# Performance work log

Measured on AMD Instinct MI355X. Metric: run time of the kernel, lower is better.

The kernel has to match this reference:

```python
import jax, jax.numpy as jnp
import numpy as np

B, L, S = 4, 1024, 1024
D_MODEL, H, DK = 1024, 16, 64  # d_model == H * DK required by the in-place writeback


def setup_inputs() -> dict:
    key = jax.random.key(0)
    ks = jax.random.split(key, 12)
    queries = jax.random.normal(ks[0], (B, L, D_MODEL), dtype=jnp.float32)
    keys = jax.random.normal(ks[1], (B, S, D_MODEL), dtype=jnp.float32)
    values = jax.random.normal(ks[2], (B, S, D_MODEL), dtype=jnp.float32)
    gate_scores = jax.random.uniform(ks[3], (B, H, DK, D_MODEL), dtype=jnp.float32)
    sc = 1.0 / np.sqrt(D_MODEL)
    W_q = jax.random.normal(ks[4], (H * DK, D_MODEL), dtype=jnp.float32) * sc
    b_q = jax.random.normal(ks[5], (H * DK,), dtype=jnp.float32) * 0.01
    W_k = jax.random.normal(ks[6], (H * DK, D_MODEL), dtype=jnp.float32) * sc
    b_k = jax.random.normal(ks[7], (H * DK,), dtype=jnp.float32) * 0.01
    W_v = jax.random.normal(ks[8], (H * DK, D_MODEL), dtype=jnp.float32) * sc
    b_v = jax.random.normal(ks[9], (H * DK,), dtype=jnp.float32) * 0.01
    W_o = jax.random.normal(ks[10], (D_MODEL, H * DK), dtype=jnp.float32) * sc
    b_o = jax.random.normal(ks[11], (D_MODEL,), dtype=jnp.float32) * 0.01
    return {"queries": queries, "keys": keys, "values": values,
            "gate_scores": gate_scores, "W_q": W_q, "b_q": b_q,
            "W_k": W_k, "b_k": b_k, "W_v": W_v, "b_v": b_v,
            "W_o": W_o, "b_o": b_o}


def reference(queries, keys, values, gate_scores, W_q, b_q, W_k, b_k, W_v, b_v, W_o, b_o):
    # Per-sample gated Q/K/V projection: W_x[b] = gate_scores[b] * W_x  (elementwise, [H,DK,Dm])
    # fused as a batched einsum instead of the per-sample Python loop.
    Wq = W_q.reshape(H, DK, D_MODEL)
    Wk = W_k.reshape(H, DK, D_MODEL)
    Wv = W_v.reshape(H, DK, D_MODEL)
    Q = jnp.einsum('blm,bhkm,hkm->blhk', queries, gate_scores, Wq) + b_q.reshape(H, DK)
    K = jnp.einsum('bsm,bhkm,hkm->bshk', keys, gate_scores, Wk) + b_k.reshape(H, DK)
    V = jnp.einsum('bsm,bhkm,hkm->bshk', values, gate_scores, Wv) + b_v.reshape(H, DK)
    # Full scaled dot-product attention (standard inner_attention)
    scale = 1.0 / jnp.sqrt(jnp.asarray(DK, Q.dtype))
    scores = jnp.einsum('blhk,bshk->bhls', Q, K) * scale
    attn = jax.nn.softmax(scores, axis=-1)
    out = jnp.einsum('bhls,bshk->blhk', attn, V).reshape(B, L, H * DK)
    out = out @ W_o.T + b_o
    return out, attn
```

## Files before the change

kernel.cpp:

```cpp
#include <hip/hip_runtime.h>
#include <math.h>

#define BB 4
#define LL 1024
#define SS 1024
#define DM 1024
#define HH 16
#define DKH 64
#define NH 1024
#define QK_ALPHA 0.1803368801f

typedef __attribute__((ext_vector_type(8))) short bf16x8;
typedef __attribute__((ext_vector_type(4))) float f32x4;
typedef unsigned short ushort_t;
typedef unsigned int uint_t;

#define MFMA16(a, b, c) __builtin_amdgcn_mfma_f32_16x16x32_bf16((a), (b), (c), 0, 0, 0)

__device__ __forceinline__ ushort_t f2b(float f) {
    union { float f; uint_t u; } x; x.f = f;
    uint_t r = x.u + 0x7fffu + ((x.u >> 16) & 1u);
    return (ushort_t)(r >> 16);
}

__device__ __forceinline__ float b2f(ushort_t v) {
    union { float f; uint_t u; } x; x.u = ((uint_t)v) << 16;
    return x.f;
}

__device__ __forceinline__ void gload_lds16(const void* g, void* l) {
    __builtin_amdgcn_global_load_lds(
        (const __attribute__((address_space(1))) unsigned int*)g,
        (__attribute__((address_space(3))) unsigned int*)l, 16, 0, 0);
}

__device__ __forceinline__ int xcd_swz(int lin, int nwg) {
    return (lin & 7) * (nwg >> 3) + (lin >> 3);
}

__device__ __forceinline__ void cvt8(const float* src, ushort_t* dst, const float* g2) {
    float4 a  = *(const float4*)(src);
    float4 b4 = *(const float4*)(src + 4);
    if (g2) {
        float4 ga = *(const float4*)(g2);
        float4 gb = *(const float4*)(g2 + 4);
        a.x *= ga.x; a.y *= ga.y; a.z *= ga.z; a.w *= ga.w;
        b4.x *= gb.x; b4.y *= gb.y; b4.z *= gb.z; b4.w *= gb.w;
    }
    uint4 o;
    o.x = f2b(a.x)  | ((uint_t)f2b(a.y)  << 16);
    o.y = f2b(a.z)  | ((uint_t)f2b(a.w)  << 16);
    o.z = f2b(b4.x) | ((uint_t)f2b(b4.y) << 16);
    o.w = f2b(b4.z) | ((uint_t)f2b(b4.w) << 16);
    *(uint4*)dst = o;
}

__global__ __launch_bounds__(256) void prep_kernel(
    const float* __restrict__ q, const float* __restrict__ k, const float* __restrict__ v,
    const float* __restrict__ gate,
    const float* __restrict__ Wq, const float* __restrict__ Wk, const float* __restrict__ Wv,
    const float* __restrict__ Wo,
    ushort_t* __restrict__ Xq, ushort_t* __restrict__ Xk, ushort_t* __restrict__ Xv,
    ushort_t* __restrict__ Gq, ushort_t* __restrict__ Gk, ushort_t* __restrict__ Gv,
    ushort_t* __restrict__ Wo2)
{
    const int XCH = 3 * 524288;
    const int GCH = 524288;
    const int WCH = 131072;
    for (int c = blockIdx.x * 256 + threadIdx.x; c < XCH + GCH + WCH; c += gridDim.x * 256) {
        if (c < XCH) {
            int r = c >> 19;
            int e = (c & 524287) * 8;
            cvt8((r == 0 ? q : r == 1 ? k : v) + e,
                 (r == 0 ? Xq : r == 1 ? Xk : Xv) + e, nullptr);
        } else if (c < XCH + GCH) {
            int e = (c - XCH) * 8;
            int nm = e & 1048575;
            const float* g2 = gate + e;
            cvt8(Wq + nm, Gq + e, g2);
            cvt8(Wk + nm, Gk + e, g2);
            cvt8(Wv + nm, Gv + e, g2);
        } else {
            int e = (c - XCH - GCH) * 8;
            cvt8(Wo + e, Wo2 + e, nullptr);
        }
    }
}

__global__ __launch_bounds__(256) void qkv_gemm(
    const ushort_t* __restrict__ Xq, const ushort_t* __restrict__ Gq, const float* __restrict__ bq,
    const ushort_t* __restrict__ Xk, const ushort_t* __restrict__ Gk, const float* __restrict__ bk,
    const ushort_t* __restrict__ Xv, const ushort_t* __restrict__ Gv, const float* __restrict__ bv,
    ushort_t* __restrict__ Qb, ushort_t* __restrict__ Kb, ushort_t* __restrict__ Vt,
    int mode)
{
    __shared__ ushort_t As[128 * 64];
    __shared__ ushort_t Bs[128 * 64];
    const int p  = xcd_swz(blockIdx.x, gridDim.x);
    const int g2 = p >> 6;
    const int r  = p & 63;
    int b, g;
    if (mode == 0)      { b = g2 / 3;  g = g2 % 3; }
    else if (mode == 1) { b = g2 >> 1; g = g2 & 1; }
    else                { b = g2;      g = 2;      }
    const size_t off = (size_t)b * 1048576;
    const ushort_t *A, *B; const float* bias; ushort_t* C; bool brow;
    if (g == 0)      { A = Xq + off; B = Gq + off; bias = bq; C = Qb + off; brow = false; }
    else if (g == 1) { A = Xk + off; B = Gk + off; bias = bk; C = Kb + off; brow = false; }
    else             { A = Gv + off; B = Xv + off; bias = bv; C = Vt + off; brow = true;  }
    const float oscale = (g == 0) ? QK_ALPHA : 1.0f;

    const int bm = (r >> 3) * 128;
    const int bn = (r & 7) * 128;
    const int tid = threadIdx.x;
    const int lane = tid & 63;
    const int w = tid >> 6;
    const int wr = w >> 1, wc = w & 1;
    const int lr = lane & 15, lk = lane >> 4;

    f32x4 acc[4][4];
    #pragma unroll
    for (int i = 0; i < 4; ++i)
        #pragma unroll
        for (int j = 0; j < 4; ++j)
            acc[i][j] = (f32x4){0.f, 0.f, 0.f, 0.f};

    for (int k0 = 0; k0 < 1024; k0 += 64) {
        #pragma unroll
        for (int pp = 0; pp < 4; ++pp) {
            int f = pp * 256 + tid;
            int row = f >> 3, seg = f & 7;
            int kb2 = (seg * 8) ^ ((row & 7) * 8);
            gload_lds16(A + (size_t)(bm + row) * 1024 + k0 + kb2,
                        (char*)As + ((pp * 256 + (w << 6)) << 4));
            gload_lds16(B + (size_t)(bn + row) * 1024 + k0 + kb2,
                        (char*)Bs + ((pp * 256 + (w << 6)) << 4));
        }
        __syncthreads();
        #pragma unroll
        for (int kk = 0; kk < 2; ++kk) {
            bf16x8 af[4], bfr[4];
            #pragma unroll
            for (int i = 0; i < 4; ++i) {
                int row = wr * 64 + i * 16 + lr;
                af[i] = *(const bf16x8*)&As[row * 64 + ((lk * 8 + kk * 32) ^ ((row & 7) * 8))];
            }
            #pragma unroll
            for (int j = 0; j < 4; ++j) {
                int row = wc * 64 + j * 16 + lr;
                bfr[j] = *(const bf16x8*)&Bs[row * 64 + ((lk * 8 + kk * 32) ^ ((row & 7) * 8))];
            }
            #pragma unroll
            for (int i = 0; i < 4; ++i)
                #pragma unroll
                for (int j = 0; j < 4; ++j)
                    acc[i][j] = MFMA16(af[i], bfr[j], acc[i][j]);
        }
        __syncthreads();
    }

    #pragma unroll
    for (int i = 0; i < 4; ++i)
        #pragma unroll
        for (int j = 0; j < 4; ++j)
            #pragma unroll
            for (int rr = 0; rr < 4; ++rr) {
                int row = bm + wr * 64 + i * 16 + lk * 4 + rr;
                int col = bn + wc * 64 + j * 16 + lr;
                float vv = (acc[i][j][rr] + bias[brow ? row : col]) * oscale;
                C[(size_t)row * 1024 + col] = f2b(vv);
            }
}

__global__ __launch_bounds__(512) void fused_attn_kernel(
    const ushort_t* __restrict__ Q, const ushort_t* __restrict__ Kmat,
    const ushort_t* __restrict__ Vt, float* __restrict__ attn,
    ushort_t* __restrict__ ctx)
{
    __shared__ ushort_t K2[2][128 * 64];
    __shared__ ushort_t V2[2][64 * 128];
    __shared__ ushort_t Ps[8 * 1024];
    const int p  = xcd_swz(blockIdx.x, gridDim.x);
    const int bh = p >> 3;
    const int b  = bh >> 4;
    const int h  = bh & 15;
    const int r0 = (p & 7) * 128;
    const int tid = threadIdx.x, lane = tid & 63, w = tid >> 6;
    const int lr = lane & 15, lk = lane >> 4;

    bf16x8 aq[2];
    {
        const ushort_t* Qrow = Q + ((size_t)b * LL + r0 + w * 16 + lr) * NH + h * DKH;
        aq[0] = *(const bf16x8*)(Qrow + lk * 8);
        aq[1] = *(const bf16x8*)(Qrow + lk * 8 + 32);
    }
    const ushort_t* Kp = Kmat + (size_t)b * SS * NH + h * DKH;
    const ushort_t* Vp = Vt + ((size_t)b * NH + h * DKH) * SS;
    ushort_t* Psw = Ps + w * 1024;

    const int srow = tid >> 3;
    const int sseg = tid & 7;
    const int skb  = (sseg * 8) ^ ((srow & 7) * 8);
    const int vrow = tid >> 4;
    const int vseg = tid & 15;
    const int vkb  = (vseg * 8) ^ ((vrow & 7) * 8);

#define STAGE_K(t, buf)                                                          \
    do {                                                                         \
        gload_lds16(Kp + (size_t)((t) * 128 + srow) * NH + skb,                  \
                    (char*)(&K2[buf][0]) + (w << 10));                           \
        gload_lds16(Kp + (size_t)((t) * 128 + 64 + srow) * NH + skb,             \
                    (char*)(&K2[buf][0]) + 8192 + (w << 10));                    \
    } while (0)
#define STAGE_V(t, buf)                                                          \
    do {                                                                         \
        gload_lds16(Vp + (size_t)vrow * SS + (t) * 128 + vkb,                    \
                    (char*)(&V2[buf][0]) + (w << 10));                           \
        gload_lds16(Vp + (size_t)(vrow + 32) * SS + (t) * 128 + vkb,             \
                    (char*)(&V2[buf][0]) + 8192 + (w << 10));                    \
    } while (0)

    float inv[4] = {0.f, 0.f, 0.f, 0.f};

    STAGE_K(0, 0);
    __syncthreads();
    for (int t = 0; t < 8; ++t) {
        const int cur = t & 1;
        if (t < 7) STAGE_K(t + 1, cur ^ 1);
        #pragma unroll
        for (int jh = 0; jh < 2; ++jh) {
            f32x4 acc[4];
            #pragma unroll
            for (int j = 0; j < 4; ++j) acc[j] = (f32x4){0.f, 0.f, 0.f, 0.f};
            #pragma unroll
            for (int kk = 0; kk < 2; ++kk)
                #pragma unroll
                for (int j = 0; j < 4; ++j) {
                    int row = jh * 64 + j * 16 + lr;
                    bf16x8 bk2 = *(const bf16x8*)&K2[cur][row * 64 + ((lk * 8 + kk * 32) ^ ((row & 7) * 8))];
                    acc[j] = MFMA16(aq[kk], bk2, acc[j]);
                }
            #pragma unroll
            for (int rr = 0; rr < 4; ++rr)
                inv[rr] += __builtin_amdgcn_exp2f(acc[0][rr]) + __builtin_amdgcn_exp2f(acc[1][rr])
                         + __builtin_amdgcn_exp2f(acc[2][rr]) + __builtin_amdgcn_exp2f(acc[3][rr]);
        }
        __syncthreads();
    }
    #pragma unroll
    for (int rr = 0; rr < 4; ++rr) {
        float s = inv[rr];
        s += __shfl_xor(s, 1);
        s += __shfl_xor(s, 2);
        s += __shfl_xor(s, 4);
        s += __shfl_xor(s, 8);
        inv[rr] = 1.0f / s;
    }

    f32x4 occ[4];
    #pragma unroll
    for (int j = 0; j < 4; ++j) occ[j] = (f32x4){0.f, 0.f, 0.f, 0.f};
    float* Ob = attn + (((size_t)b * HH + h) * LL + r0 + w * 16) * SS;
    const int erow = lane >> 3;
    const int eseg = lane & 7;

    STAGE_K(0, 0);
    STAGE_V(0, 0);
    __syncthreads();
    for (int t = 0; t < 8; ++t) {
        const int cur = t & 1;
        if (t < 7) { STAGE_K(t + 1, cur ^ 1); STAGE_V(t + 1, cur ^ 1); }
        #pragma unroll
        for (int jh = 0; jh < 2; ++jh) {
            f32x4 acc[4];
            #pragma unroll
            for (int j = 0; j < 4; ++j) acc[j] = (f32x4){0.f, 0.f, 0.f, 0.f};
            #pragma unroll
            for (int kk = 0; kk < 2; ++kk)
                #pragma unroll
                for (int j = 0; j < 4; ++j) {
                    int row = jh * 64 + j * 16 + lr;
                    bf16x8 bk2 = *(const bf16x8*)&K2[cur][row * 64 + ((lk * 8 + kk * 32) ^ ((row & 7) * 8))];
                    acc[j] = MFMA16(aq[kk], bk2, acc[j]);
                }
            #pragma unroll
            for (int j = 0; j < 4; ++j)
                #pragma unroll
                for (int rr = 0; rr < 4; ++rr) {
                    int ql = lk * 4 + rr;
                    float pv = __builtin_amdgcn_exp2f(acc[j][rr]) * inv[rr];
                    Psw[ql * 64 + ((j * 16 + lr) ^ ((ql & 7) * 8))] = f2b(pv);
                }
            #pragma unroll
            for (int kk = 0; kk < 2; ++kk) {
                bf16x8 pa = *(const bf16x8*)&Psw[lr * 64 + ((kk * 32 + lk * 8) ^ ((lr & 7) * 8))];
                #pragma unroll
                for (int j = 0; j < 4; ++j) {
                    int row = j * 16 + lr;
                    bf16x8 bv2 = *(const bf16x8*)&V2[cur][row * 128 + ((jh * 64 + kk * 32 + lk * 8) ^ ((row & 7) * 8))];
                    occ[j] = MFMA16(pa, bv2, occ[j]);
                }
            }
            float* Obt = Ob + t * 128 + jh * 64;
            #pragma unroll
            for (int hh = 0; hh < 2; ++hh) {
                int rl = erow + hh * 8;
                bf16x8 p8 = *(const bf16x8*)&Psw[rl * 64 + ((eseg * 8) ^ ((rl & 7) * 8))];
                float4 o0 = make_float4(b2f((ushort_t)p8[0]), b2f((ushort_t)p8[1]),
                                        b2f((ushort_t)p8[2]), b2f((ushort_t)p8[3]));
                float4 o1 = make_float4(b2f((ushort_t)p8[4]), b2f((ushort_t)p8[5]),
                                        b2f((ushort_t)p8[6]), b2f((ushort_t)p8[7]));
                *(float4*)(Obt + (size_t)rl * SS + eseg * 8) = o0;
                *(float4*)(Obt + (size_t)rl * SS + eseg * 8 + 4) = o1;
            }
        }
        __syncthreads();
    }

    #pragma unroll
    for (int j = 0; j < 4; ++j)
        #pragma unroll
        for (int rr = 0; rr < 4; ++rr)
            ctx[((size_t)b * LL + r0 + w * 16 + lk * 4 + rr) * NH + h * DKH + j * 16 + lr]
                = f2b(occ[j][rr]);
#undef STAGE_K
#undef STAGE_V
}

__global__ __launch_bounds__(256) void out_gemm(
    const ushort_t* __restrict__ A, const ushort_t* __restrict__ B,
    const float* __restrict__ bias, float* __restrict__ C)
{
    __shared__ ushort_t As[128 * 64];
    __shared__ ushort_t Bs[64 * 64];
    const int p  = xcd_swz(blockIdx.x, gridDim.x);
    const int bm = (p >> 4) * 128;
    const int bn = (p & 15) * 64;
    const int tid = threadIdx.x;
    const int lane = tid & 63;
    const int w = tid >> 6;
    const int wr = w >> 1, wc = w & 1;
    const int lr = lane & 15, lk = lane >> 4;

    f32x4 acc[4][2];
    #pragma unroll
    for (int i = 0; i < 4; ++i)
        #pragma unroll
        for (int j = 0; j < 2; ++j)
            acc[i][j] = (f32x4){0.f, 0.f, 0.f, 0.f};

    for (int k0 = 0; k0 < 1024; k0 += 64) {
        #pragma unroll
        for (int pp = 0; pp < 4; ++pp) {
            int f = pp * 256 + tid;
            int row = f >> 3, seg = f & 7;
            int kb2 = (seg * 8) ^ ((row & 7) * 8);
            gload_lds16(A + (size_t)(bm + row) * 1024 + k0 + kb2,
                        (char*)As + ((pp * 256 + (w << 6)) << 4));
        }
        #pragma unroll
        for (int pp = 0; pp < 2; ++pp) {
            int f = pp * 256 + tid;
            int row = f >> 3, seg = f & 7;
            int kb2 = (seg * 8) ^ ((row & 7) * 8);
            gload_lds16(B + (size_t)(bn + row) * 1024 + k0 + kb2,
                        (char*)Bs + ((pp * 256 + (w << 6)) << 4));
        }
        __syncthreads();
        #pragma unroll
        for (int kk = 0; kk < 2; ++kk) {
            bf16x8 af[4], bfr[2];
            #pragma unroll
            for (int i = 0; i < 4; ++i) {
                int row = wr * 64 + i * 16 + lr;
                af[i] = *(const bf16x8*)&As[row * 64 + ((lk * 8 + kk * 32) ^ ((row & 7) * 8))];
            }
            #pragma unroll
            for (int j = 0; j < 2; ++j) {
                int row = wc * 32 + j * 16 + lr;
                bfr[j] = *(const bf16x8*)&Bs[row * 64 + ((lk * 8 + kk * 32) ^ ((row & 7) * 8))];
            }
            #pragma unroll
            for (int i = 0; i < 4; ++i)
                #pragma unroll
                for (int j = 0; j < 2; ++j)
                    acc[i][j] = MFMA16(af[i], bfr[j], acc[i][j]);
        }
        __syncthreads();
    }

    #pragma unroll
    for (int i = 0; i < 4; ++i)
        #pragma unroll
        for (int j = 0; j < 2; ++j)
            #pragma unroll
            for (int rr = 0; rr < 4; ++rr) {
                int row = bm + wr * 64 + i * 16 + lk * 4 + rr;
                int col = bn + wc * 32 + j * 16 + lr;
                C[(size_t)row * DM + col] = acc[i][j][rr] + bias[col];
            }
}

extern "C" void kernel_launch(void* const* d_in, const int* in_sizes, int n_in,
                              void* d_out, int out_size, void* d_ws, size_t ws_size,
                              hipStream_t stream)
{
    const float* queries = (const float*)d_in[0];
    const float* keys    = (const float*)d_in[1];
    const float* values  = (const float*)d_in[2];
    const float* gate    = (const float*)d_in[3];
    const float* W_q     = (const float*)d_in[4];
    const float* b_q     = (const float*)d_in[5];
    const float* W_k     = (const float*)d_in[6];
    const float* b_k     = (const float*)d_in[7];
    const float* W_v     = (const float*)d_in[8];
    const float* b_v     = (const float*)d_in[9];
    const float* W_o     = (const float*)d_in[10];
    const float* b_o     = (const float*)d_in[11];

    float* out  = (float*)d_out;
    float* attn = out + (size_t)BB * LL * DM;

    char* ws = (char*)d_ws;
    const size_t U = (size_t)8 << 20;
    ushort_t* Xq = (ushort_t*)(ws);
    ushort_t* Xk = (ushort_t*)(ws + 1 * U);
    ushort_t* Xv = (ushort_t*)(ws + 2 * U);
    ushort_t* Gq = (ushort_t*)(ws + 3 * U);
    ushort_t* Gk = (ushort_t*)(ws + 4 * U);
    ushort_t* Gv = (ushort_t*)(ws + 5 * U);
    ushort_t* Vt = (ushort_t*)(ws + 6 * U);
    const bool big = ws_size >= 9 * U + ((size_t)2 << 20);
    ushort_t *Qb, *Kb, *Wo2;
    if (big) { Qb = (ushort_t*)(ws + 7 * U); Kb = (ushort_t*)(ws + 8 * U); Wo2 = (ushort_t*)(ws + 9 * U); }
    else     { Qb = Xv; Kb = Gv; Wo2 = (ushort_t*)(ws + 7 * U); }
    ushort_t* ctx = Xq;

    dim3 blk(256, 1, 1);
    prep_kernel<<<2048, blk, 0, stream>>>(queries, keys, values, gate,
                                          W_q, W_k, W_v, W_o,
                                          Xq, Xk, Xv, Gq, Gk, Gv, Wo2);
    if (big) {
        qkv_gemm<<<768, blk, 0, stream>>>(Xq, Gq, b_q, Xk, Gk, b_k,
                                          Xv, Gv, b_v, Qb, Kb, Vt, 0);
    } else {
        qkv_gemm<<<256, blk, 0, stream>>>(Xq, Gq, b_q, Xk, Gk, b_k,
                                          Xv, Gv, b_v, Qb, Kb, Vt, 2);
        qkv_gemm<<<512, blk, 0, stream>>>(Xq, Gq, b_q, Xk, Gk, b_k,
                                          Xv, Gv, b_v, Qb, Kb, Vt, 1);
    }
    fused_attn_kernel<<<512, dim3(512, 1, 1), 0, stream>>>(Qb, Kb, Vt, attn, ctx);
    out_gemm<<<512, blk, 0, stream>>>(ctx, Wo2, b_o, out);
}
```

Baseline: 171.1 us.

## Split softmax row-sum pass into separate parallel rowsum and inverse kernels

Moves the first pass of the two-pass softmax (computing exp-sums of QK^T per row) out of the fused attention kernel into a dedicated rowsum kernel with 4096 blocks over 128x128 tiles, followed by a small kernel that reduces the partials and inverts them. The fused kernel then just loads the precomputed inverse sums. This is meant to remove the serial first pass from the 512-block attention kernel, which has limited parallelism, and spread it over many more blocks. In exchange it adds two launches and a round trip of partial sums through global memory, and it reuses the Gq/Gk workspace buffers after the QKV GEMM has finished with them.

Measured after the change: 193.0 us. 1.13x slower.

```diff
diff --git a/kernel.cpp b/kernel.cpp
--- a/kernel.cpp
+++ b/kernel.cpp
@@ -172,10 +172,96 @@
             }
 }
 
+__global__ __launch_bounds__(256) void rowsum_kernel(
+    const ushort_t* __restrict__ Qb, const ushort_t* __restrict__ Kb,
+    float* __restrict__ partial)
+{
+    __shared__ ushort_t Qs[128 * 64];
+    __shared__ ushort_t Ks[128 * 64];
+    const int p  = xcd_swz(blockIdx.x, gridDim.x);
+    const int bh = p >> 6;
+    const int r  = p & 63;
+    const int l0 = (r >> 3) * 128;
+    const int st = r & 7;
+    const int s0 = st * 128;
+    const int b = bh >> 4, h = bh & 15;
+    const int tid = threadIdx.x, lane = tid & 63, w = tid >> 6;
+    const int wr = w >> 1, wc = w & 1;
+    const int lr = lane & 15, lk = lane >> 4;
+
+    const ushort_t* Qp = Qb + (size_t)b * LL * NH + h * DKH;
+    const ushort_t* Kp = Kb + (size_t)b * SS * NH + h * DKH;
+
+    #pragma unroll
+    for (int pp = 0; pp < 4; ++pp) {
+        int f = pp * 256 + tid;
+        int row = f >> 3, seg = f & 7;
+        int kb2 = (seg * 8) ^ ((row & 7) * 8);
+        gload_lds16(Qp + (size_t)(l0 + row) * NH + kb2,
+                    (char*)Qs + ((pp * 256 + (w << 6)) << 4));
+        gload_lds16(Kp + (size_t)(s0 + row) * NH + kb2,
+                    (char*)Ks + ((pp * 256 + (w << 6)) << 4));
+    }
+    __syncthreads();
+
+    f32x4 acc[4][4];
+    #pragma unroll
+    for (int i = 0; i < 4; ++i)
+        #pragma unroll
+        for (int j = 0; j < 4; ++j)
+            acc[i][j] = (f32x4){0.f, 0.f, 0.f, 0.f};
+    #pragma unroll
+    for (int kk = 0; kk < 2; ++kk) {
+        bf16x8 af[4], bfr[4];
+        #pragma unroll
+        for (int i = 0; i < 4; ++i) {
+            int row = wr * 64 + i * 16 + lr;
+            af[i] = *(const bf16x8*)&Qs[row * 64 + ((lk * 8 + kk * 32) ^ ((row & 7) * 8))];
+        }
+        #pragma unroll
+        for (int j = 0; j < 4; ++j) {
+            int row = wc * 64 + j * 16 + lr;
+            bfr[j] = *(const bf16x8*)&Ks[row * 64 + ((lk * 8 + kk * 32) ^ ((row & 7) * 8))];
+        }
+        #pragma unroll
+        for (int i = 0; i < 4; ++i)
+            #pragma unroll
+            for (int j = 0; j < 4; ++j)
+                acc[i][j] = MFMA16(af[i], bfr[j], acc[i][j]);
+    }
+    #pragma unroll
+    for (int i = 0; i < 4; ++i)
+        #pragma unroll
+        for (int rr = 0; rr < 4; ++rr) {
+            float s = __builtin_amdgcn_exp2f(acc[i][0][rr]) + __builtin_amdgcn_exp2f(acc[i][1][rr])
+                    + __builtin_amdgcn_exp2f(acc[i][2][rr]) + __builtin_amdgcn_exp2f(acc[i][3][rr]);
+            s += __shfl_xor(s, 1);
+            s += __shfl_xor(s, 2);
+            s += __shfl_xor(s, 4);
+            s += __shfl_xor(s, 8);
+            if (lr == 0) {
+                int row = l0 + wr * 64 + i * 16 + lk * 4 + rr;
+                partial[((size_t)bh * 16 + st * 2 + wc) * 1024 + row] = s;
+            }
+        }
+}
+
+__global__ __launch_bounds__(256) void inv_kernel(
+    const float* __restrict__ partial, float* __restrict__ invbuf)
+{
+    int i = blockIdx.x * 256 + threadIdx.x;
+    int bh = i >> 10, l = i & 1023;
+    float s = 0.f;
+    #pragma unroll
+    for (int c = 0; c < 16; ++c)
+        s += partial[((size_t)bh * 16 + c) * 1024 + l];
+    invbuf[i] = 1.0f / s;
+}
+
 __global__ __launch_bounds__(512) void fused_attn_kernel(
     const ushort_t* __restrict__ Q, const ushort_t* __restrict__ Kmat,
-    const ushort_t* __restrict__ Vt, float* __restrict__ attn,
-    ushort_t* __restrict__ ctx)
+    const ushort_t* __restrict__ Vt, const float* __restrict__ invbuf,
+    float* __restrict__ attn, ushort_t* __restrict__ ctx)
 {
     __shared__ ushort_t K2[2][128 * 64];
     __shared__ ushort_t V2[2][64 * 128];
@@ -197,6 +283,11 @@
     const ushort_t* Kp = Kmat + (size_t)b * SS * NH + h * DKH;
     const ushort_t* Vp = Vt + ((size_t)b * NH + h * DKH) * SS;
     ushort_t* Psw = Ps + w * 1024;
+
+    float inv[4];
+    #pragma unroll
+    for (int rr = 0; rr < 4; ++rr)
+        inv[rr] = invbuf[bh * 1024 + r0 + w * 16 + lk * 4 + rr];
 
     const int srow = tid >> 3;
     const int sseg = tid & 7;
@@ -220,43 +311,6 @@
                     (char*)(&V2[buf][0]) + 8192 + (w << 10));                    \
     } while (0)
 
-    float inv[4] = {0.f, 0.f, 0.f, 0.f};
-
-    STAGE_K(0, 0);
-    __syncthreads();
-    for (int t = 0; t < 8; ++t) {
-        const int cur = t & 1;
-        if (t < 7) STAGE_K(t + 1, cur ^ 1);
-        #pragma unroll
-        for (int jh = 0; jh < 2; ++jh) {
-            f32x4 acc[4];
-            #pragma unroll
-            for (int j = 0; j < 4; ++j) acc[j] = (f32x4){0.f, 0.f, 0.f, 0.f};
-            #pragma unroll
-            for (int kk = 0; kk < 2; ++kk)
-                #pragma unroll
-                for (int j = 0; j < 4; ++j) {
-                    int row = jh * 64 + j * 16 + lr;
-                    bf16x8 bk2 = *(const bf16x8*)&K2[cur][row * 64 + ((lk * 8 + kk * 32) ^ ((row & 7) * 8))];
-                    acc[j] = MFMA16(aq[kk], bk2, acc[j]);
-                }
-            #pragma unroll
-            for (int rr = 0; rr < 4; ++rr)
-                inv[rr] += __builtin_amdgcn_exp2f(acc[0][rr]) + __builtin_amdgcn_exp2f(acc[1][rr])
-                         + __builtin_amdgcn_exp2f(acc[2][rr]) + __builtin_amdgcn_exp2f(acc[3][rr]);
-        }
-        __syncthreads();
-    }
-    #pragma unroll
-    for (int rr = 0; rr < 4; ++rr) {
-        float s = inv[rr];
-        s += __shfl_xor(s, 1);
-        s += __shfl_xor(s, 2);
-        s += __shfl_xor(s, 4);
-        s += __shfl_xor(s, 8);
-        inv[rr] = 1.0f / s;
-    }
-
     f32x4 occ[4];
     #pragma unroll
     for (int j = 0; j < 4; ++j) occ[j] = (f32x4){0.f, 0.f, 0.f, 0.f};
@@ -435,6 +489,8 @@
     if (big) { Qb = (ushort_t*)(ws + 7 * U); Kb = (ushort_t*)(ws + 8 * U); Wo2 = (ushort_t*)(ws + 9 * U); }
     else     { Qb = Xv; Kb = Gv; Wo2 = (ushort_t*)(ws + 7 * U); }
     ushort_t* ctx = Xq;
+    float* partial = (float*)Gq;
+    float* invbuf  = (float*)Gk;
 
     dim3 blk(256, 1, 1);
     prep_kernel<<<2048, blk, 0, stream>>>(queries, keys, values, gate,
@@ -449,6 +505,8 @@
         qkv_gemm<<<512, blk, 0, stream>>>(Xq, Gq, b_q, Xk, Gk, b_k,
                                           Xv, Gv, b_v, Qb, Kb, Vt, 1);
     }
-    fused_attn_kernel<<<512, dim3(512, 1, 1), 0, stream>>>(Qb, Kb, Vt, attn, ctx);
+    rowsum_kernel<<<4096, blk, 0, stream>>>(Qb, Kb, partial);
+    inv_kernel<<<256, blk, 0, stream>>>(partial, invbuf);
+    fused_attn_kernel<<<512, dim3(512, 1, 1), 0, stream>>>(Qb, Kb, Vt, invbuf, attn, ctx);
     out_gemm<<<512, blk, 0, stream>>>(ctx, Wo2, b_o, out);
 }
```
